# Performance work log

Measured on AMD Instinct MI355X. Metric: run time of the kernel, lower is better.

Reference implementation:

```python
import jax, jax.numpy as jnp
import numpy as np

L = 4; B = 128; S = 128; N = B * S; E = 262144
IN = 64; HID = 128; PE = 16; HEADS = 4; DK = HID // HEADS; OUT = 10


def setup_inputs() -> dict:
    key = jax.random.key(0)
    ks = iter(jax.random.split(key, 64))
    def nrm(shape, scale=1.0):
        return jax.random.normal(next(ks), shape, jnp.float32) * scale
    inp = {
        'x': nrm((N, IN)),
        'pe': nrm((N, PE)),
        'edge_attr': nrm((E, HID)),
        'sph': jax.random.uniform(next(ks), (B, 1, S, S), jnp.float32),
        'node_w': nrm((IN, HID - PE), 0.05), 'node_b': jnp.zeros((HID - PE,), jnp.float32),
        'pe_w': nrm((PE, PE), 0.05), 'pe_b': jnp.zeros((PE,), jnp.float32),
        'conv_Aw': nrm((L, HID, HID), 0.05), 'conv_Ab': jnp.zeros((L, HID), jnp.float32),
        'conv_Bw': nrm((L, HID, HID), 0.05), 'conv_Bb': jnp.zeros((L, HID), jnp.float32),
        'conv_Cw': nrm((L, HID, HID), 0.05), 'conv_Cb': jnp.zeros((L, HID), jnp.float32),
        'conv_Dw': nrm((L, HID, HID), 0.05), 'conv_Db': jnp.zeros((L, HID), jnp.float32),
        'conv_Ew': nrm((L, HID, HID), 0.05), 'conv_Eb': jnp.zeros((L, HID), jnp.float32),
        'bnx_g': jnp.ones((L, HID), jnp.float32), 'bnx_b': jnp.zeros((L, HID), jnp.float32),
        'bne_g': jnp.ones((L, HID), jnp.float32), 'bne_b': jnp.zeros((L, HID), jnp.float32),
        'attn_w': nrm((4, HID, HID), 0.05), 'attn_b': jnp.zeros((4, HID), jnp.float32),
        'mlp1_w': nrm((HID, HID // 2), 0.05), 'mlp1_b': jnp.zeros((HID // 2,), jnp.float32),
        'mlp2_w': nrm((HID // 2, HID // 4), 0.05), 'mlp2_b': jnp.zeros((HID // 4,), jnp.float32),
        'mlp3_w': nrm((HID // 4, OUT), 0.05), 'mlp3_b': jnp.zeros((OUT,), jnp.float32),
        'edge_index': jax.random.randint(next(ks), (2, E), 0, N, dtype=jnp.int32),
        'batch': jnp.repeat(jnp.arange(B, dtype=jnp.int32), S),  # equal-size graphs, sorted
    }
    return inp


def _bn(v, g, b):
    # BatchNorm1d in training mode (batch statistics), eps=1e-5
    mu = v.mean(0)
    var = jnp.mean((v - mu) ** 2, 0)
    return g * (v - mu) * jax.lax.rsqrt(var + 1e-5) + b


def _forward(x, pe, edge_attr, sph, node_w, node_b, pe_w, pe_b,
             conv_Aw, conv_Ab, conv_Bw, conv_Bb, conv_Cw, conv_Cb,
             conv_Dw, conv_Db, conv_Ew, conv_Eb,
             bnx_g, bnx_b, bne_g, bne_b, attn_w, attn_b,
             mlp1_w, mlp1_b, mlp2_w, mlp2_b, mlp3_w, mlp3_b,
             edge_index, batch):
    src, dst = edge_index[0], edge_index[1]  # message j->i: index = dst
    h = jnp.concatenate([x @ node_w + node_b, pe @ pe_w + pe_b], axis=-1)  # [N, HID]
    e = edge_attr
    inv_sqrt_dk = np.float32(1.0 / np.sqrt(DK))
    for l in range(L):
        # ---- GatedGCNConv (residual, aggr='add' with sigmoid-gated normalization) ----
        Ax = h @ conv_Aw[l] + conv_Ab[l]
        Bx = h @ conv_Bw[l] + conv_Bb[l]
        Ce = e @ conv_Cw[l] + conv_Cb[l]
        Dx = h @ conv_Dw[l] + conv_Db[l]
        Ex = h @ conv_Ew[l] + conv_Eb[l]
        e_ij = Dx[dst] + Ex[src] + Ce               # [E, HID] pre-sigmoid edge feature
        sigma = jax.nn.sigmoid(e_ij)
        num = jax.ops.segment_sum(sigma * Bx[src], dst, num_segments=N)
        den = jax.ops.segment_sum(sigma, dst, num_segments=N)
        h_new = Ax + num / (den + 1e-6)
        h = jax.nn.relu(_bn(h_new, bnx_g[l], bnx_b[l])) + h
        e = jax.nn.relu(_bn(e_ij, bne_g[l], bne_b[l])) + e
        # ---- dense MHA with sph score bias (to_dense_batch == reshape, equal-size graphs) ----
        xd = h.reshape(B, S, HID)
        q = (xd @ attn_w[0] + attn_b[0]).reshape(B, S, HEADS, DK).transpose(0, 2, 1, 3)
        k = (xd @ attn_w[1] + attn_b[1]).reshape(B, S, HEADS, DK).transpose(0, 2, 1, 3)
        v = (xd @ attn_w[2] + attn_b[2]).reshape(B, S, HEADS, DK).transpose(0, 2, 1, 3)
        scores = jnp.einsum('bhsd,bhtd->bhst', q, k) * inv_sqrt_dk
        p = jax.nn.softmax(scores * sph, axis=-1)
        o = jnp.einsum('bhst,bhtd->bhsd', p, v).transpose(0, 2, 1, 3).reshape(B, S, HID)
        h = (o @ attn_w[3] + attn_b[3]).reshape(N, HID)
    # global mean pool over each graph
    g = jax.ops.segment_sum(h, batch, num_segments=B) / np.float32(S)
    g = jax.nn.relu(g @ mlp1_w + mlp1_b)
    g = jax.nn.relu(g @ mlp2_w + mlp2_b)
    return g @ mlp3_w + mlp3_b  # [B, OUT]


def reference(x, pe, edge_attr, sph, node_w, node_b, pe_w, pe_b,
              conv_Aw, conv_Ab, conv_Bw, conv_Bb, conv_Cw, conv_Cb,
              conv_Dw, conv_Db, conv_Ew, conv_Eb,
              bnx_g, bnx_b, bne_g, bne_b, attn_w, attn_b,
              mlp1_w, mlp1_b, mlp2_w, mlp2_b, mlp3_w, mlp3_b,
              edge_index, batch):
    return _forward(x, pe, edge_attr, sph, node_w, node_b, pe_w, pe_b,
                    conv_Aw, conv_Ab, conv_Bw, conv_Bb, conv_Cw, conv_Cb,
                    conv_Dw, conv_Db, conv_Ew, conv_Eb,
                    bnx_g, bnx_b, bne_g, bne_b, attn_w, attn_b,
                    mlp1_w, mlp1_b, mlp2_w, mlp2_b, mlp3_w, mlp3_b,
                    edge_index, batch)
```

## Files before the change

kernel.cpp:

```cpp
#include <hip/hip_runtime.h>
#include <math.h>

#define L_LAYERS 4
#define B_G 128
#define S_G 128
#define N_N 16384
#define E_E 262144
#define IN_F 64
#define HID 128
#define PE_F 16
#define HEADS 4
#define DK 32
#define OUT_F 10

typedef __bf16 bf16x8 __attribute__((ext_vector_type(8)));
typedef float f32x4 __attribute__((ext_vector_type(4)));

struct Sel4 { float* o[4]; const float* b[4]; int slot[4]; };
struct WSrc24 { const float* w[24]; };

__global__ void zero_int_kernel(int* __restrict__ p, int n) {
    int i = blockIdx.x * 256 + threadIdx.x;
    if (i < n) p[i] = 0;
}

__global__ void hist_kernel(const int* __restrict__ dst, int* __restrict__ deg) {
    int e = blockIdx.x * 256 + threadIdx.x;
    if (e < E_E) atomicAdd(&deg[dst[e]], 1);
}

__global__ __launch_bounds__(1024) void scan_kernel(const int* __restrict__ deg,
                                                    int* __restrict__ row_ptr,
                                                    int* __restrict__ cursor) {
    __shared__ int lds[1024];
    int tid = threadIdx.x;
    int base = tid * 16;
    int d[16];
    int s = 0;
#pragma unroll
    for (int i = 0; i < 16; i++) { d[i] = deg[base + i]; s += d[i]; }
    lds[tid] = s;
    __syncthreads();
    for (int off = 1; off < 1024; off <<= 1) {
        int v = (tid >= off) ? lds[tid - off] : 0;
        __syncthreads();
        lds[tid] += v;
        __syncthreads();
    }
    int run = lds[tid] - s;
#pragma unroll
    for (int i = 0; i < 16; i++) {
        row_ptr[base + i] = run;
        cursor[base + i] = run;
        run += d[i];
    }
    if (tid == 1023) row_ptr[N_N] = run;
}

__global__ void scatter_kernel(const int* __restrict__ src, const int* __restrict__ dst,
                               int* __restrict__ cursor, int* __restrict__ perm,
                               int* __restrict__ ssrc, int* __restrict__ sdst) {
    int e = blockIdx.x * 256 + threadIdx.x;
    if (e >= E_E) return;
    int dd = dst[e];
    int pos = atomicAdd(&cursor[dd], 1);
    perm[pos] = e;
    ssrc[pos] = src[e];
    sdst[pos] = dd;
}

__global__ __launch_bounds__(256) void pack_w_kernel(WSrc24 ws, __bf16* __restrict__ Whi,
                                                     __bf16* __restrict__ Wlo) {
    int m = blockIdx.x;
    const float* W = ws.w[m];
    int tid = threadIdx.x;
    for (int i = 0; i < 64; i++) {
        int p = i * 256 + tid;
        int j = p & 7, lane = (p >> 3) & 63, kc = (p >> 9) & 3, nt = p >> 11;
        int k = kc * 32 + (lane >> 4) * 8 + j;
        int n = nt * 16 + (lane & 15);
        float w = W[k * 128 + n];
        __bf16 h = (__bf16)w;
        Whi[(long)m * 16384 + p] = h;
        Wlo[(long)m * 16384 + p] = (__bf16)(w - (float)h);
    }
}

__global__ void embed_kernel(const float* __restrict__ x, const float* __restrict__ pe,
                             const float* __restrict__ node_w, const float* __restrict__ node_b,
                             const float* __restrict__ pe_w, const float* __restrict__ pe_b,
                             float* __restrict__ h) {
    int idx = blockIdx.x * 256 + threadIdx.x;
    if (idx >= N_N * HID) return;
    int i = idx >> 7, c = idx & 127;
    float acc;
    if (c < 112) {
        acc = node_b[c];
        const float* xr = x + (long)i * IN_F;
        for (int k = 0; k < IN_F; k++) acc += xr[k] * node_w[k * 112 + c];
    } else {
        int cc = c - 112;
        acc = pe_b[cc];
        const float* pr = pe + (long)i * PE_F;
        for (int k = 0; k < PE_F; k++) acc += pr[k] * pe_w[k * PE_F + cc];
    }
    h[idx] = acc;
}

template <int MODE>
__global__ __launch_bounds__(256) void mfma_gemm_kernel(
    const float* __restrict__ A, const int* __restrict__ perm,
    const __bf16* __restrict__ Whi, const __bf16* __restrict__ Wlo, Sel4 sel,
    const float* __restrict__ Dx, const float* __restrict__ Ex,
    const int* __restrict__ sdst, const int* __restrict__ ssrc,
    float* __restrict__ stats_acc) {
    __shared__ float sred[1024];
    int tid = threadIdx.x;
    int lane = tid & 63, wave = tid >> 6;
    int l15 = lane & 15, quad = lane >> 4;
    long rowBase = (long)blockIdx.x * 64 + wave * 16;
    int y = blockIdx.y;
    float* out = sel.o[y];
    const float* bias = sel.b[y];
    const bf16x8* whv = (const bf16x8*)(Whi + (long)sel.slot[y] * 16384);
    const bf16x8* wlv = (const bf16x8*)(Wlo + (long)sel.slot[y] * 16384);

    long arow = rowBase + l15;
    if (MODE == 1 && perm) arow = perm[arow];
    const float* Ap = A + arow * 128 + quad * 8;

    f32x4 acc[8];
#pragma unroll
    for (int t = 0; t < 8; t++) acc[t] = (f32x4){0.f, 0.f, 0.f, 0.f};

#pragma unroll
    for (int kc = 0; kc < 4; kc++) {
        float4 a0 = *(const float4*)(Ap + kc * 32);
        float4 a1 = *(const float4*)(Ap + kc * 32 + 4);
        float f[8] = {a0.x, a0.y, a0.z, a0.w, a1.x, a1.y, a1.z, a1.w};
        bf16x8 ahi, alo;
#pragma unroll
        for (int j = 0; j < 8; j++) {
            __bf16 hh = (__bf16)f[j];
            ahi[j] = hh;
            alo[j] = (__bf16)(f[j] - (float)hh);
        }
#pragma unroll
        for (int nt = 0; nt < 8; nt++) {
            bf16x8 bhi = whv[(nt * 4 + kc) * 64 + lane];
            bf16x8 blo = wlv[(nt * 4 + kc) * 64 + lane];
            acc[nt] = __builtin_amdgcn_mfma_f32_16x16x32_bf16(ahi, blo, acc[nt], 0, 0, 0);
            acc[nt] = __builtin_amdgcn_mfma_f32_16x16x32_bf16(alo, bhi, acc[nt], 0, 0, 0);
            acc[nt] = __builtin_amdgcn_mfma_f32_16x16x32_bf16(ahi, bhi, acc[nt], 0, 0, 0);
        }
    }

    int sd[4], ss[4];
    if (MODE == 1) {
#pragma unroll
        for (int r = 0; r < 4; r++) {
            long row = rowBase + quad * 4 + r;
            sd[r] = sdst[row];
            ss[r] = ssrc[row];
        }
    }
    float csum[8], csq[8];
#pragma unroll
    for (int nt = 0; nt < 8; nt++) { csum[nt] = 0.f; csq[nt] = 0.f; }

#pragma unroll
    for (int nt = 0; nt < 8; nt++) {
        int c = nt * 16 + l15;
        float bb = bias[c];
#pragma unroll
        for (int r = 0; r < 4; r++) {
            long row = rowBase + quad * 4 + r;
            float v = acc[nt][r] + bb;
            if (MODE == 1) v += Dx[(long)sd[r] * 128 + c] + Ex[(long)ss[r] * 128 + c];
            out[row * 128 + c] = v;
            if (MODE == 1) { csum[nt] += v; csq[nt] += v * v; }
        }
    }

    if (MODE == 1) {
#pragma unroll
        for (int nt = 0; nt < 8; nt++) {
            float s = csum[nt];
            s += __shfl_xor(s, 16); s += __shfl_xor(s, 32);
            float q = csq[nt];
            q += __shfl_xor(q, 16); q += __shfl_xor(q, 32);
            if (quad == 0) {
                sred[wave * 256 + nt * 16 + l15] = s;
                sred[wave * 256 + 128 + nt * 16 + l15] = q;
            }
        }
        __syncthreads();
        if (tid < 256) {
            float v = sred[tid] + sred[256 + tid] + sred[512 + tid] + sred[768 + tid];
            atomicAdd(&stats_acc[tid], v);
        }
    }
}

__global__ void ebn_finalize_kernel(const float* __restrict__ acc, float invM,
                                    float* __restrict__ stat) {
    int c = threadIdx.x;
    float mu = acc[c] * invM;
    float var = acc[128 + c] * invM - mu * mu;
    stat[c] = mu;
    stat[128 + c] = rsqrtf(var + 1e-5f);
}

__global__ __launch_bounds__(256) void bn_stats_kernel(const float* __restrict__ v, long M,
                                                       float* __restrict__ partial) {
    __shared__ float lds[256];
    int tid = threadIdx.x;
    int c = tid & 127, half = tid >> 7;
    float sum = 0.f, sq = 0.f;
    for (long r = (long)blockIdx.x * 2 + half; r < M; r += (long)gridDim.x * 2) {
        float x = v[r * 128 + c];
        sum += x; sq += x * x;
    }
    lds[tid] = sum;
    __syncthreads();
    if (half == 0) sum += lds[tid + 128];
    __syncthreads();
    lds[tid] = sq;
    __syncthreads();
    if (half == 0) {
        sq += lds[tid + 128];
        partial[(long)blockIdx.x * 256 + c] = sum;
        partial[(long)blockIdx.x * 256 + 128 + c] = sq;
    }
}

__global__ void bn_finalize_kernel(const float* __restrict__ partial, int nblk, float invM,
                                   float* __restrict__ stat) {
    int c = threadIdx.x;
    float s = 0.f, q = 0.f;
    for (int i = 0; i < nblk; i++) {
        s += partial[i * 256 + c];
        q += partial[i * 256 + 128 + c];
    }
    float mu = s * invM;
    float var = q * invM - mu * mu;
    stat[c] = mu;
    stat[128 + c] = rsqrtf(var + 1e-5f);
}

__global__ void bn_apply_res_kernel(const float* __restrict__ vin, const float* __restrict__ stat,
                                    const float* __restrict__ g, const float* __restrict__ b,
                                    float* __restrict__ io, long M4) {
    long idx = (long)blockIdx.x * 256 + threadIdx.x;
    if (idx >= M4) return;
    int c4 = (idx & 31) << 2;
    float4 x = ((const float4*)vin)[idx];
    float4 res = ((float4*)io)[idx];
    float xv[4] = {x.x, x.y, x.z, x.w};
    float rv[4] = {res.x, res.y, res.z, res.w};
    float o[4];
#pragma unroll
    for (int t = 0; t < 4; t++) {
        int c = c4 + t;
        float y = g[c] * (xv[t] - stat[c]) * stat[128 + c] + b[c];
        o[t] = fmaxf(y, 0.f) + rv[t];
    }
    ((float4*)io)[idx] = make_float4(o[0], o[1], o[2], o[3]);
}

__global__ __launch_bounds__(128) void agg_bn_kernel(
    const float* __restrict__ eij, const float* __restrict__ Bx, const float* __restrict__ Ax,
    const int* __restrict__ row_ptr, const int* __restrict__ ssrc,
    const float* __restrict__ estat, const float* __restrict__ g, const float* __restrict__ b,
    const float* __restrict__ eold, const int* __restrict__ perm,
    float* __restrict__ e_out, float* __restrict__ hnew) {
    int i = blockIdx.x, c = threadIdx.x;
    int s0 = row_ptr[i], s1 = row_ptr[i + 1];
    float mu = estat[c], rs = estat[128 + c], gg = g[c], bb = b[c];
    float num = 0.f, den = 0.f;
    for (int j = s0; j < s1; j++) {
        float x = eij[(long)j * 128 + c];
        float sig = 1.f / (1.f + __expf(-x));
        num += sig * Bx[(long)ssrc[j] * 128 + c];
        den += sig;
        long er = perm ? (long)perm[j] : (long)j;
        float old = eold[er * 128 + c];
        float y = fmaxf(gg * (x - mu) * rs + bb, 0.f) + old;
        e_out[(long)j * 128 + c] = y;
    }
    long idx = (long)i * 128 + c;
    hnew[idx] = Ax[idx] + num / (den + 1e-6f);
}

__global__ __launch_bounds__(256) void attn_kernel(const float* __restrict__ q,
                                                   const float* __restrict__ k,
                                                   const float* __restrict__ v,
                                                   const float* __restrict__ sph,
                                                   float* __restrict__ o) {
    __shared__ float k_lds[128 * 32];
    __shared__ float v_lds[128 * 32];
    int b = blockIdx.x >> 2, hd = blockIdx.x & 3;
    int tid = threadIdx.x;

    for (int i = tid; i < 1024; i += 256) {
        int t = i >> 3, d4 = i & 7;
        long gidx = (long)(b * 128 + t) * 32 + hd * 8 + d4;
        ((float4*)k_lds)[t * 8 + d4] = ((const float4*)k)[gidx];
        ((float4*)v_lds)[t * 8 + d4] = ((const float4*)v)[gidx];
    }
    __syncthreads();

    int s = tid >> 1, t0 = (tid & 1) * 64;
    float4 qreg[8];
    long qbase = (long)(b * 128 + s) * 32 + hd * 8;
#pragma unroll
    for (int j = 0; j < 8; j++) qreg[j] = ((const float4*)q)[qbase + j];
    const float* sphrow = sph + ((long)b * 128 + s) * 128 + t0;
    const float inv_sqrt_dk = 0.17677669529663687f;

    float p[64];
#pragma unroll
    for (int i = 0; i < 64; i++) {
        const float4* kr = (const float4*)&k_lds[(t0 + i) * 32];
        float acc = 0.f;
#pragma unroll
        for (int j = 0; j < 8; j++) {
            float4 kv = kr[j];
            acc += qreg[j].x * kv.x + qreg[j].y * kv.y + qreg[j].z * kv.z + qreg[j].w * kv.w;
        }
        p[i] = acc * inv_sqrt_dk * sphrow[i];
    }
    float m = -1e30f;
#pragma unroll
    for (int i = 0; i < 64; i++) m = fmaxf(m, p[i]);
    m = fmaxf(m, __shfl_xor(m, 1));
    float l = 0.f;
#pragma unroll
    for (int i = 0; i < 64; i++) {
        p[i] = __expf(p[i] - m);
        l += p[i];
    }
    l += __shfl_xor(l, 1);
    float invl = 1.f / l;

    float part[32];
#pragma unroll
    for (int d = 0; d < 32; d++) part[d] = 0.f;
#pragma unroll
    for (int i = 0; i < 64; i++) {
        float pv = p[i] * invl;
        const float4* vr = (const float4*)&v_lds[(t0 + i) * 32];
#pragma unroll
        for (int j = 0; j < 8; j++) {
            float4 vv = vr[j];
            part[4 * j + 0] += pv * vv.x;
            part[4 * j + 1] += pv * vv.y;
            part[4 * j + 2] += pv * vv.z;
            part[4 * j + 3] += pv * vv.w;
        }
    }
    int halfw = tid & 1;
    float outv[16];
#pragma unroll
    for (int d = 0; d < 32; d++) {
        float tot = part[d] + __shfl_xor(part[d], 1);
        if ((d >> 4) == halfw) outv[d & 15] = tot;
    }
    long obase = (long)(b * 128 + s) * 32 + hd * 8 + halfw * 4;
#pragma unroll
    for (int j = 0; j < 4; j++)
        ((float4*)o)[obase + j] = make_float4(outv[4 * j], outv[4 * j + 1], outv[4 * j + 2], outv[4 * j + 3]);
}

__global__ __launch_bounds__(128) void pool_mlp_kernel(
    const float* __restrict__ h, const float* __restrict__ w1, const float* __restrict__ b1,
    const float* __restrict__ w2, const float* __restrict__ b2, const float* __restrict__ w3,
    const float* __restrict__ b3, float* __restrict__ out) {
    __shared__ float g[128], m1[64], m2[32];
    int b = blockIdx.x, tid = threadIdx.x;
    const float* hb = h + (long)b * 128 * 128;
    float s = 0.f;
    for (int r = 0; r < 128; r++) s += hb[r * 128 + tid];
    g[tid] = s * (1.f / 128.f);
    __syncthreads();
    if (tid < 64) {
        float a = b1[tid];
        for (int kk = 0; kk < 128; kk++) a += g[kk] * w1[kk * 64 + tid];
        m1[tid] = fmaxf(a, 0.f);
    }
    __syncthreads();
    if (tid < 32) {
        float a = b2[tid];
        for (int kk = 0; kk < 64; kk++) a += m1[kk] * w2[kk * 32 + tid];
        m2[tid] = fmaxf(a, 0.f);
    }
    __syncthreads();
    if (tid < 10) {
        float a = b3[tid];
        for (int kk = 0; kk < 32; kk++) a += m2[kk] * w3[kk * 10 + tid];
        out[b * 10 + tid] = a;
    }
}

extern "C" void kernel_launch(void* const* d_in, const int* in_sizes, int n_in,
                              void* d_out, int out_size, void* d_ws, size_t ws_size,
                              hipStream_t stream) {
    (void)in_sizes; (void)n_in; (void)out_size;
    const float* x        = (const float*)d_in[0];
    const float* pe       = (const float*)d_in[1];
    const float* edge_attr= (const float*)d_in[2];
    const float* sph      = (const float*)d_in[3];
    const float* node_w   = (const float*)d_in[4];
    const float* node_b   = (const float*)d_in[5];
    const float* pe_w     = (const float*)d_in[6];
    const float* pe_b     = (const float*)d_in[7];
    const float* conv_Aw  = (const float*)d_in[8];
    const float* conv_Ab  = (const float*)d_in[9];
    const float* conv_Bw  = (const float*)d_in[10];
    const float* conv_Bb  = (const float*)d_in[11];
    const float* conv_Cw  = (const float*)d_in[12];
    const float* conv_Cb  = (const float*)d_in[13];
    const float* conv_Dw  = (const float*)d_in[14];
    const float* conv_Db  = (const float*)d_in[15];
    const float* conv_Ew  = (const float*)d_in[16];
    const float* conv_Eb  = (const float*)d_in[17];
    const float* bnx_g    = (const float*)d_in[18];
    const float* bnx_b    = (const float*)d_in[19];
    const float* bne_g    = (const float*)d_in[20];
    const float* bne_b    = (const float*)d_in[21];
    const float* attn_w   = (const float*)d_in[22];
    const float* attn_b   = (const float*)d_in[23];
    const float* mlp1_w   = (const float*)d_in[24];
    const float* mlp1_b   = (const float*)d_in[25];
    const float* mlp2_w   = (const float*)d_in[26];
    const float* mlp2_b   = (const float*)d_in[27];
    const float* mlp3_w   = (const float*)d_in[28];
    const float* mlp3_b   = (const float*)d_in[29];
    const int*   eidx     = (const int*)d_in[30];
    const int* esrc = eidx;
    const int* edst = eidx + E_E;
    float* out = (float*)d_out;

    float* f = (float*)d_ws;
    float* h      = f; f += (long)N_N * HID;
    float* hnew   = f; f += (long)N_N * HID;
    float* Ax     = f; f += (long)N_N * HID;
    float* Bx     = f; f += (long)N_N * HID;
    float* Dx     = f; f += (long)N_N * HID;
    float* Ex     = f; f += (long)N_N * HID;
    float* e      = f; f += (long)E_E * HID;
    float* eij    = f; f += (long)E_E * HID;
    float* partial= f; f += 512 * 256;
    float* bnxs   = f; f += 256;
    float* bnes   = f; f += 256;
    float* ebn_acc= f; f += 256;
    __bf16* Whi = (__bf16*)f;
    __bf16* Wlo = Whi + 24 * 16384;
    int* ip = (int*)(Wlo + 24 * 16384);
    int* deg     = ip; ip += N_N;
    int* row_ptr = ip; ip += N_N + 1;
    int* cursor  = ip; ip += N_N;
    int* perm    = ip; ip += E_E;
    int* ssrc    = ip; ip += E_E;
    int* sdst    = ip; ip += E_E;
    size_t need = (size_t)((char*)ip - (char*)d_ws);
    if (ws_size < need) return;

    WSrc24 wsrc;
    for (int l = 0; l < L_LAYERS; l++) {
        wsrc.w[l * 5 + 0] = conv_Aw + l * 16384;
        wsrc.w[l * 5 + 1] = conv_Bw + l * 16384;
        wsrc.w[l * 5 + 2] = conv_Cw + l * 16384;
        wsrc.w[l * 5 + 3] = conv_Dw + l * 16384;
        wsrc.w[l * 5 + 4] = conv_Ew + l * 16384;
    }
    for (int m = 0; m < 4; m++) wsrc.w[20 + m] = attn_w + m * 16384;
    pack_w_kernel<<<24, 256, 0, stream>>>(wsrc, Whi, Wlo);

    zero_int_kernel<<<(N_N + 255) / 256, 256, 0, stream>>>(deg, N_N);
    hist_kernel<<<E_E / 256, 256, 0, stream>>>(edst, deg);
    scan_kernel<<<1, 1024, 0, stream>>>(deg, row_ptr, cursor);
    scatter_kernel<<<E_E / 256, 256, 0, stream>>>(esrc, edst, cursor, perm, ssrc, sdst);

    embed_kernel<<<N_N * HID / 256, 256, 0, stream>>>(x, pe, node_w, node_b, pe_w, pe_b, h);

    for (int l = 0; l < L_LAYERS; l++) {
        zero_int_kernel<<<1, 256, 0, stream>>>((int*)ebn_acc, 256);

        Sel4 selN;
        selN.o[0] = Ax; selN.b[0] = conv_Ab + l * 128; selN.slot[0] = l * 5 + 0;
        selN.o[1] = Bx; selN.b[1] = conv_Bb + l * 128; selN.slot[1] = l * 5 + 1;
        selN.o[2] = Dx; selN.b[2] = conv_Db + l * 128; selN.slot[2] = l * 5 + 3;
        selN.o[3] = Ex; selN.b[3] = conv_Eb + l * 128; selN.slot[3] = l * 5 + 4;
        mfma_gemm_kernel<0><<<dim3(N_N / 64, 4), 256, 0, stream>>>(
            h, nullptr, Whi, Wlo, selN, nullptr, nullptr, nullptr, nullptr, nullptr);

        const float* Asrc = (l == 0) ? edge_attr : e;
        const int* permA = (l == 0) ? perm : nullptr;
        Sel4 selE;
        selE.o[0] = eij; selE.b[0] = conv_Cb + l * 128; selE.slot[0] = l * 5 + 2;
        selE.o[1] = selE.o[2] = selE.o[3] = eij;
        selE.b[1] = selE.b[2] = selE.b[3] = selE.b[0];
        selE.slot[1] = selE.slot[2] = selE.slot[3] = selE.slot[0];
        mfma_gemm_kernel<1><<<dim3(E_E / 64, 1), 256, 0, stream>>>(
            Asrc, permA, Whi, Wlo, selE, Dx, Ex, sdst, ssrc, ebn_acc);

        ebn_finalize_kernel<<<1, 128, 0, stream>>>(ebn_acc, 1.f / E_E, bnes);

        const float* eoldSrc = (l == 0) ? edge_attr : e;
        const int* permE = (l == 0) ? perm : nullptr;
        agg_bn_kernel<<<N_N, 128, 0, stream>>>(eij, Bx, Ax, row_ptr, ssrc, bnes,
                                               bne_g + l * 128, bne_b + l * 128,
                                               eoldSrc, permE, e, hnew);

        bn_stats_kernel<<<128, 256, 0, stream>>>(hnew, (long)N_N, partial);
        bn_finalize_kernel<<<1, 128, 0, stream>>>(partial, 128, 1.f / N_N, bnxs);
        bn_apply_res_kernel<<<N_N * 32 / 256, 256, 0, stream>>>(
            hnew, bnxs, bnx_g + l * 128, bnx_b + l * 128, h, (long)N_N * 32);

        Sel4 selQ;
        selQ.o[0] = Ax; selQ.b[0] = attn_b;       selQ.slot[0] = 20;
        selQ.o[1] = Bx; selQ.b[1] = attn_b + 128; selQ.slot[1] = 21;
        selQ.o[2] = Dx; selQ.b[2] = attn_b + 256; selQ.slot[2] = 22;
        selQ.o[3] = Dx; selQ.b[3] = attn_b + 256; selQ.slot[3] = 22;
        mfma_gemm_kernel<0><<<dim3(N_N / 64, 3), 256, 0, stream>>>(
            h, nullptr, Whi, Wlo, selQ, nullptr, nullptr, nullptr, nullptr, nullptr);

        attn_kernel<<<B_G * HEADS, 256, 0, stream>>>(Ax, Bx, Dx, sph, Ex);

        Sel4 selP;
        selP.o[0] = h; selP.b[0] = attn_b + 384; selP.slot[0] = 23;
        selP.o[1] = selP.o[2] = selP.o[3] = h;
        selP.b[1] = selP.b[2] = selP.b[3] = selP.b[0];
        selP.slot[1] = selP.slot[2] = selP.slot[3] = selP.slot[0];
        mfma_gemm_kernel<0><<<dim3(N_N / 64, 1), 256, 0, stream>>>(
            Ex, nullptr, Whi, Wlo, selP, nullptr, nullptr, nullptr, nullptr, nullptr);
    }

    pool_mlp_kernel<<<B_G, 128, 0, stream>>>(h, mlp1_w, mlp1_b, mlp2_w, mlp2_b, mlp3_w, mlp3_b, out);
}
```

Measured before the change: 1.862 ms.

## Make MFMA GEMM persistent with register-resident weight slices per wave

The GEMM kernel is restructured so each wave owns two 16-column output tiles and keeps its bf16 hi/lo weight fragments in registers. Blocks then loop grid-stride over 16-row tiles instead of each block handling 64 rows across all 128 columns. This removes repeated weight loads per tile and cuts the edge-BN atomic reductions to once per persistent block. In exchange, all four waves load the same A rows, so A traffic per block rises fourfold (served mostly from cache), and there are fewer independent accumulators per wave for hiding MFMA latency.

```diff
diff --git a/kernel.cpp b/kernel.cpp
--- a/kernel.cpp
+++ b/kernel.cpp
@@ -108,97 +108,102 @@
 }
 
 template <int MODE>
-__global__ __launch_bounds__(256) void mfma_gemm_kernel(
+__global__ __launch_bounds__(256) void mfma_gemm_ws_kernel(
     const float* __restrict__ A, const int* __restrict__ perm,
     const __bf16* __restrict__ Whi, const __bf16* __restrict__ Wlo, Sel4 sel,
     const float* __restrict__ Dx, const float* __restrict__ Ex,
     const int* __restrict__ sdst, const int* __restrict__ ssrc,
-    float* __restrict__ stats_acc) {
-    __shared__ float sred[1024];
+    float* __restrict__ stats_acc, int ntiles) {
+    __shared__ float sred[256];
     int tid = threadIdx.x;
     int lane = tid & 63, wave = tid >> 6;
     int l15 = lane & 15, quad = lane >> 4;
-    long rowBase = (long)blockIdx.x * 64 + wave * 16;
     int y = blockIdx.y;
     float* out = sel.o[y];
     const float* bias = sel.b[y];
     const bf16x8* whv = (const bf16x8*)(Whi + (long)sel.slot[y] * 16384);
     const bf16x8* wlv = (const bf16x8*)(Wlo + (long)sel.slot[y] * 16384);
 
-    long arow = rowBase + l15;
-    if (MODE == 1 && perm) arow = perm[arow];
-    const float* Ap = A + arow * 128 + quad * 8;
-
-    f32x4 acc[8];
-#pragma unroll
-    for (int t = 0; t < 8; t++) acc[t] = (f32x4){0.f, 0.f, 0.f, 0.f};
-
-#pragma unroll
-    for (int kc = 0; kc < 4; kc++) {
-        float4 a0 = *(const float4*)(Ap + kc * 32);
-        float4 a1 = *(const float4*)(Ap + kc * 32 + 4);
-        float f[8] = {a0.x, a0.y, a0.z, a0.w, a1.x, a1.y, a1.z, a1.w};
-        bf16x8 ahi, alo;
-#pragma unroll
-        for (int j = 0; j < 8; j++) {
-            __bf16 hh = (__bf16)f[j];
-            ahi[j] = hh;
-            alo[j] = (__bf16)(f[j] - (float)hh);
+    bf16x8 bh[2][4], bl[2][4];
+#pragma unroll
+    for (int ntl = 0; ntl < 2; ntl++)
+#pragma unroll
+        for (int kc = 0; kc < 4; kc++) {
+            int fi = ((2 * wave + ntl) * 4 + kc) * 64 + lane;
+            bh[ntl][kc] = whv[fi];
+            bl[ntl][kc] = wlv[fi];
         }
-#pragma unroll
-        for (int nt = 0; nt < 8; nt++) {
-            bf16x8 bhi = whv[(nt * 4 + kc) * 64 + lane];
-            bf16x8 blo = wlv[(nt * 4 + kc) * 64 + lane];
-            acc[nt] = __builtin_amdgcn_mfma_f32_16x16x32_bf16(ahi, blo, acc[nt], 0, 0, 0);
-            acc[nt] = __builtin_amdgcn_mfma_f32_16x16x32_bf16(alo, bhi, acc[nt], 0, 0, 0);
-            acc[nt] = __builtin_amdgcn_mfma_f32_16x16x32_bf16(ahi, bhi, acc[nt], 0, 0, 0);
+
+    int c0 = (2 * wave) * 16 + l15, c1 = (2 * wave + 1) * 16 + l15;
+    float bias0 = bias[c0], bias1 = bias[c1];
+
+    float csum[2] = {0.f, 0.f}, csq[2] = {0.f, 0.f};
+
+    for (int t = blockIdx.x; t < ntiles; t += gridDim.x) {
+        long rowA = (long)t * 16 + l15;
+        if (MODE == 1 && perm) rowA = perm[rowA];
+        const float* Ap = A + rowA * 128 + quad * 8;
+
+        f32x4 acc0 = (f32x4){0.f, 0.f, 0.f, 0.f};
+        f32x4 acc1 = (f32x4){0.f, 0.f, 0.f, 0.f};
+#pragma unroll
+        for (int kc = 0; kc < 4; kc++) {
+            float4 a0 = *(const float4*)(Ap + kc * 32);
+            float4 a1 = *(const float4*)(Ap + kc * 32 + 4);
+            float fv[8] = {a0.x, a0.y, a0.z, a0.w, a1.x, a1.y, a1.z, a1.w};
+            bf16x8 ahi, alo;
+#pragma unroll
+            for (int j = 0; j < 8; j++) {
+                __bf16 hh = (__bf16)fv[j];
+                ahi[j] = hh;
+                alo[j] = (__bf16)(fv[j] - (float)hh);
+            }
+            acc0 = __builtin_amdgcn_mfma_f32_16x16x32_bf16(ahi, bl[0][kc], acc0, 0, 0, 0);
+            acc1 = __builtin_amdgcn_mfma_f32_16x16x32_bf16(ahi, bl[1][kc], acc1, 0, 0, 0);
+            acc0 = __builtin_amdgcn_mfma_f32_16x16x32_bf16(alo, bh[0][kc], acc0, 0, 0, 0);
+            acc1 = __builtin_amdgcn_mfma_f32_16x16x32_bf16(alo, bh[1][kc], acc1, 0, 0, 0);
+            acc0 = __builtin_amdgcn_mfma_f32_16x16x32_bf16(ahi, bh[0][kc], acc0, 0, 0, 0);
+            acc1 = __builtin_amdgcn_mfma_f32_16x16x32_bf16(ahi, bh[1][kc], acc1, 0, 0, 0);
         }
-    }
-
-    int sd[4], ss[4];
+
+        long rb = (long)t * 16 + quad * 4;
+        if (MODE == 1) {
+            int sd[4], ss[4];
+#pragma unroll
+            for (int r = 0; r < 4; r++) { sd[r] = sdst[rb + r]; ss[r] = ssrc[rb + r]; }
+#pragma unroll
+            for (int r = 0; r < 4; r++) {
+                float v0 = acc0[r] + bias0 + Dx[(long)sd[r] * 128 + c0] + Ex[(long)ss[r] * 128 + c0];
+                float v1 = acc1[r] + bias1 + Dx[(long)sd[r] * 128 + c1] + Ex[(long)ss[r] * 128 + c1];
+                out[(rb + r) * 128 + c0] = v0;
+                out[(rb + r) * 128 + c1] = v1;
+                csum[0] += v0; csq[0] += v0 * v0;
+                csum[1] += v1; csq[1] += v1 * v1;
+            }
+        } else {
+#pragma unroll
+            for (int r = 0; r < 4; r++) {
+                out[(rb + r) * 128 + c0] = acc0[r] + bias0;
+                out[(rb + r) * 128 + c1] = acc1[r] + bias1;
+            }
+        }
+    }
+
     if (MODE == 1) {
 #pragma unroll
-        for (int r = 0; r < 4; r++) {
-            long row = rowBase + quad * 4 + r;
-            sd[r] = sdst[row];
-            ss[r] = ssrc[row];
-        }
-    }
-    float csum[8], csq[8];
-#pragma unroll
-    for (int nt = 0; nt < 8; nt++) { csum[nt] = 0.f; csq[nt] = 0.f; }
-
-#pragma unroll
-    for (int nt = 0; nt < 8; nt++) {
-        int c = nt * 16 + l15;
-        float bb = bias[c];
-#pragma unroll
-        for (int r = 0; r < 4; r++) {
-            long row = rowBase + quad * 4 + r;
-            float v = acc[nt][r] + bb;
-            if (MODE == 1) v += Dx[(long)sd[r] * 128 + c] + Ex[(long)ss[r] * 128 + c];
-            out[row * 128 + c] = v;
-            if (MODE == 1) { csum[nt] += v; csq[nt] += v * v; }
-        }
-    }
-
-    if (MODE == 1) {
-#pragma unroll
-        for (int nt = 0; nt < 8; nt++) {
-            float s = csum[nt];
+        for (int ntl = 0; ntl < 2; ntl++) {
+            float s = csum[ntl];
             s += __shfl_xor(s, 16); s += __shfl_xor(s, 32);
-            float q = csq[nt];
+            float q = csq[ntl];
             q += __shfl_xor(q, 16); q += __shfl_xor(q, 32);
             if (quad == 0) {
-                sred[wave * 256 + nt * 16 + l15] = s;
-                sred[wave * 256 + 128 + nt * 16 + l15] = q;
+                int c = (2 * wave + ntl) * 16 + l15;
+                sred[c] = s;
+                sred[128 + c] = q;
             }
         }
         __syncthreads();
-        if (tid < 256) {
-            float v = sred[tid] + sred[256 + tid] + sred[512 + tid] + sred[768 + tid];
-            atomicAdd(&stats_acc[tid], v);
-        }
+        atomicAdd(&stats_acc[tid], sred[tid]);
     }
 }
 
@@ -492,8 +497,8 @@
         selN.o[1] = Bx; selN.b[1] = conv_Bb + l * 128; selN.slot[1] = l * 5 + 1;
         selN.o[2] = Dx; selN.b[2] = conv_Db + l * 128; selN.slot[2] = l * 5 + 3;
         selN.o[3] = Ex; selN.b[3] = conv_Eb + l * 128; selN.slot[3] = l * 5 + 4;
-        mfma_gemm_kernel<0><<<dim3(N_N / 64, 4), 256, 0, stream>>>(
-            h, nullptr, Whi, Wlo, selN, nullptr, nullptr, nullptr, nullptr, nullptr);
+        mfma_gemm_ws_kernel<0><<<dim3(256, 4), 256, 0, stream>>>(
+            h, nullptr, Whi, Wlo, selN, nullptr, nullptr, nullptr, nullptr, nullptr, N_N / 16);
 
         const float* Asrc = (l == 0) ? edge_attr : e;
         const int* permA = (l == 0) ? perm : nullptr;
@@ -502,8 +507,8 @@
         selE.o[1] = selE.o[2] = selE.o[3] = eij;
         selE.b[1] = selE.b[2] = selE.b[3] = selE.b[0];
         selE.slot[1] = selE.slot[2] = selE.slot[3] = selE.slot[0];
-        mfma_gemm_kernel<1><<<dim3(E_E / 64, 1), 256, 0, stream>>>(
-            Asrc, permA, Whi, Wlo, selE, Dx, Ex, sdst, ssrc, ebn_acc);
+        mfma_gemm_ws_kernel<1><<<dim3(1024, 1), 256, 0, stream>>>(
+            Asrc, permA, Whi, Wlo, selE, Dx, Ex, sdst, ssrc, ebn_acc, E_E / 16);
 
         ebn_finalize_kernel<<<1, 128, 0, stream>>>(ebn_acc, 1.f / E_E, bnes);
 
@@ -523,8 +528,8 @@
         selQ.o[1] = Bx; selQ.b[1] = attn_b + 128; selQ.slot[1] = 21;
         selQ.o[2] = Dx; selQ.b[2] = attn_b + 256; selQ.slot[2] = 22;
         selQ.o[3] = Dx; selQ.b[3] = attn_b + 256; selQ.slot[3] = 22;
-        mfma_gemm_kernel<0><<<dim3(N_N / 64, 3), 256, 0, stream>>>(
-            h, nullptr, Whi, Wlo, selQ, nullptr, nullptr, nullptr, nullptr, nullptr);
+        mfma_gemm_ws_kernel<0><<<dim3(340, 3), 256, 0, stream>>>(
+            h, nullptr, Whi, Wlo, selQ, nullptr, nullptr, nullptr, nullptr, nullptr, N_N / 16);
 
         attn_kernel<<<B_G * HEADS, 256, 0, stream>>>(Ax, Bx, Dx, sph, Ex);
 
@@ -533,8 +538,8 @@
         selP.o[1] = selP.o[2] = selP.o[3] = h;
         selP.b[1] = selP.b[2] = selP.b[3] = selP.b[0];
         selP.slot[1] = selP.slot[2] = selP.slot[3] = selP.slot[0];
-        mfma_gemm_kernel<0><<<dim3(N_N / 64, 1), 256, 0, stream>>>(
-            Ex, nullptr, Whi, Wlo, selP, nullptr, nullptr, nullptr, nullptr, nullptr);
+        mfma_gemm_ws_kernel<0><<<dim3(512, 1), 256, 0, stream>>>(
+            Ex, nullptr, Whi, Wlo, selP, nullptr, nullptr, nullptr, nullptr, nullptr, N_N / 16);
     }
 
     pool_mlp_kernel<<<B_G, 128, 0, stream>>>(h, mlp1_w, mlp1_b, mlp2_w, mlp2_b, mlp3_w, mlp3_b, out);
```

Result: no change. 1.851 ms (-0.6%).
